# Performance work log

Measured on AMD Instinct MI355X. Metric: run time of the kernel, lower is better.

## Reference

```python
import jax, jax.numpy as jnp
import numpy as np

K = 4096          # in_features
N = 11008         # out_features
GROUP = 128       # scale group size along K
PACK = 16
BATCH, SEQ = 2, 4096


def setup_inputs() -> dict:
    key = jax.random.key(0)
    k1, k2, k3, k4 = jax.random.split(key, 4)
    x = jax.random.normal(k1, (BATCH, SEQ, K), dtype=jnp.float16)
    # valid ternary codes in {0,1,2} encoding w = code - 1 in {-1,0,+1}
    codes = jax.random.randint(k2, (K, N), 0, 3, dtype=jnp.int32)
    codes = codes.reshape(K // PACK, PACK, N)
    shifts = (2 * jnp.arange(PACK, dtype=jnp.int32))[None, :, None]
    packed_weight = jnp.sum(codes << shifts, axis=1).astype(jnp.int32)  # (K//16, N)
    scales = (jax.random.uniform(k3, (K // GROUP, N), dtype=jnp.float32) * 0.1 + 0.01).astype(jnp.float16)
    bias = (jax.random.normal(k4, (N,), dtype=jnp.float32) * 0.01).astype(jnp.float16)
    return {"x": x, "packed_weight": packed_weight, "scales": scales, "bias": bias}


def _dequant(packed_weight, scales):
    # unpack 16 two-bit codes per int32 along K
    shifts = (2 * jnp.arange(PACK, dtype=jnp.int32))[None, :, None]
    codes = (packed_weight[:, None, :] >> shifts) & 3        # (K//16, 16, N)
    Kp = packed_weight.shape[0] * PACK
    Nn = packed_weight.shape[1]
    w = (codes.astype(jnp.float16) - jnp.float16(1.0)).reshape(Kp, Nn)  # ternary {-1,0,1}
    scale_full = jnp.repeat(scales, GROUP, axis=0)            # (K, N) group-wise gamma
    return w * scale_full


def reference(x, packed_weight, scales, bias):
    Kp = packed_weight.shape[0] * PACK
    Nn = packed_weight.shape[1]
    w = _dequant(packed_weight, scales)                       # (K, N) fp16
    x2 = x.reshape(-1, Kp).astype(jnp.float16)                # (M, K)
    out = jnp.dot(x2, w, preferred_element_type=jnp.float32).astype(jnp.float16)
    out = out + bias
    return out.reshape(*x.shape[:-1], Nn)
```

## Files before the change

kernel.cpp:

```cpp
#include <hip/hip_runtime.h>
#include <stdint.h>

#define K_DIM 4096
#define N_DIM 11008
#define M_DIM 8192
#define BM 256
#define BN 128
#define BK 64
#define NSLAB (K_DIM / BK)
#define NBN (N_DIM / BN)
#define NBM (M_DIM / BM)
#define NWG (NBN * NBM)
#define ABUF (BM * BK)

#define FBM 128
#define FBK 32
#define FASTRIDE 32
#define FBSTRIDE 40

typedef _Float16 half8   __attribute__((ext_vector_type(8)));
typedef _Float16 half2v  __attribute__((ext_vector_type(2)));
typedef float    floatx4 __attribute__((ext_vector_type(4)));

#define WS_NEEDED ((size_t)M_DIM * K_DIM * 2)

__device__ __forceinline__ void async_lds16(const void* g, void* l) {
    __builtin_amdgcn_global_load_lds(
        (const __attribute__((address_space(1))) uint32_t*)g,
        (__attribute__((address_space(3))) uint32_t*)l, 16, 0, 0);
}

__global__ __launch_bounds__(256) void cvt_a(const float* __restrict__ x,
                                             _Float16* __restrict__ xh) {
    const size_t i = ((size_t)blockIdx.x * 256 + threadIdx.x) * 8;
    const float4 a = *(const float4*)(x + i);
    const float4 b = *(const float4*)(x + i + 4);
    half8 h;
    h[0] = (_Float16)a.x; h[1] = (_Float16)a.y; h[2] = (_Float16)a.z; h[3] = (_Float16)a.w;
    h[4] = (_Float16)b.x; h[5] = (_Float16)b.y; h[6] = (_Float16)b.z; h[7] = (_Float16)b.w;
    *(half8*)(xh + i) = h;
}

__global__ __launch_bounds__(512, 4) void ternary_gemm_p2(
    const _Float16* __restrict__ xh,
    const int*   __restrict__ pw,
    const float* __restrict__ scales,
    const float* __restrict__ bias,
    float*       __restrict__ out)
{
    __shared__ __align__(16) _Float16 lds_a[2 * ABUF];
    __shared__ __align__(16) _Float16 lds_b[BN * BK];

    const int tid  = threadIdx.x;
    const int lane = tid & 63;
    const int w    = tid >> 6;

    const int bid = blockIdx.x;
    const int swz = (bid & 7) * (NWG / 8) + (bid >> 3);
    const int m0 = (swz / NBN) * BM;
    const int n0 = (swz % NBN) * BN;

    const int band = (w & 3) * 64;
    const int wn   = (w >> 2) * 64;

    const _Float16* ga[4];
    int laOff[4];
    #pragma unroll
    for (int i = 0; i < 4; ++i) {
        const int idx = tid + i * 512;
        const int row = idx >> 3;
        const int c   = idx & 7;
        ga[i]    = xh + (size_t)(m0 + row) * K_DIM + ((c ^ (row & 7)) * 8);
        laOff[i] = idx * 8;
    }

    const int nb = tid >> 2;
    const int kp = tid & 3;
    const int* pwp = pw + (size_t)kp * N_DIM + n0 + nb;
    const float* scp = scales + n0 + nb;
    const int s7 = nb & 7;
    const int cA = (kp * 2 + 0) ^ s7;
    const int cB = (kp * 2 + 1) ^ s7;
    _Float16* bl = lds_b + nb * BK;

    floatx4 acc[4][4];
    #pragma unroll
    for (int i = 0; i < 4; ++i)
        #pragma unroll
        for (int j = 0; j < 4; ++j)
            acc[i][j] = floatx4{0.f, 0.f, 0.f, 0.f};

    const int lr = lane & 15;
    const int g  = lane >> 4;
    const int x7 = lr & 7;

    int aoff[4], boff[4];
    #pragma unroll
    for (int t = 0; t < 4; ++t) {
        aoff[t] = (band + t * 16 + lr) * BK;
        boff[t] = (wn   + t * 16 + lr) * BK;
    }

    auto stage_a = [&](int t, int buf) {
        #pragma unroll
        for (int i = 0; i < 4; ++i)
            async_lds16(ga[i] + t * BK, lds_a + buf * ABUF + laOff[i]);
    };
    auto stage_b = [&](uint32_t v, float scf) {
        _Float16 sh = (_Float16)scf;
        uint32_t sbits = (uint32_t)__builtin_bit_cast(unsigned short, sh);
        uint32_t tmpl = sbits | (((sbits >> 8) ^ 0x80u) << 24);
        uint32_t q[8];
        #pragma unroll
        for (int j = 0; j < 8; ++j) {
            uint32_t t4 = (v >> (4 * j)) & 0xFu;
            uint32_t sp = (t4 | (t4 << 14)) & 0x00030003u;
            uint32_t sel = ((sp & 0x00010001u) << 1) | ((0x00030003u - sp) << 8);
            q[j] = __builtin_amdgcn_perm(tmpl, tmpl, sel);
        }
        *(uint4*)(bl + cA * 8) = make_uint4(q[0], q[1], q[2], q[3]);
        *(uint4*)(bl + cB * 8) = make_uint4(q[4], q[5], q[6], q[7]);
    };

    stage_a(0, 0);
    uint32_t pv0 = (uint32_t)pwp[0];
    float    sv0 = scp[0];
    uint32_t pv1 = (uint32_t)pwp[(size_t)4 * N_DIM];
    float    sv1 = scp[0];

    for (int t = 0; t < NSLAB; ++t) {
        const int cur = t & 1;

        if (t + 1 < NSLAB) stage_a(t + 1, cur ^ 1);
        uint32_t pv2 = 0; float sv2 = 0.f;
        if (t + 2 < NSLAB) {
            pv2 = (uint32_t)pwp[(size_t)(t + 2) * 4 * N_DIM];
            sv2 = scp[(size_t)((t + 2) >> 1) * N_DIM];
        }
        stage_b(pv0, sv0);

        if (t + 2 < NSLAB)      asm volatile("s_waitcnt vmcnt(6)" ::: "memory");
        else if (t + 1 < NSLAB) asm volatile("s_waitcnt vmcnt(4)" ::: "memory");
        else                    asm volatile("s_waitcnt vmcnt(0)" ::: "memory");
        asm volatile("s_waitcnt lgkmcnt(0)" ::: "memory");
        __builtin_amdgcn_sched_barrier(0);
        __builtin_amdgcn_s_barrier();

        const _Float16* Ab = lds_a + cur * ABUF;
        __builtin_amdgcn_s_setprio(1);
        #pragma unroll
        for (int h = 0; h < 2; ++h) {
            const int co = ((h * 4 + g) ^ x7) * 8;
            half8 af[4], bfr[4];
            #pragma unroll
            for (int tt = 0; tt < 4; ++tt) {
                af[tt]  = *(const half8*)&Ab[aoff[tt] + co];
                bfr[tt] = *(const half8*)&lds_b[boff[tt] + co];
            }
            #pragma unroll
            for (int mt = 0; mt < 4; ++mt)
                #pragma unroll
                for (int nt = 0; nt < 4; ++nt)
                    acc[mt][nt] = __builtin_amdgcn_mfma_f32_16x16x32_f16(
                        af[mt], bfr[nt], acc[mt][nt], 0, 0, 0);
        }
        __builtin_amdgcn_s_setprio(0);

        asm volatile("s_waitcnt lgkmcnt(0)" ::: "memory");
        __builtin_amdgcn_sched_barrier(0);
        __builtin_amdgcn_s_barrier();

        pv0 = pv1; sv0 = sv1; pv1 = pv2; sv1 = sv2;
    }

    float bv[4];
    #pragma unroll
    for (int nt = 0; nt < 4; ++nt) bv[nt] = bias[n0 + wn + nt * 16 + lr];

    const int rbase = g * 4;
    #pragma unroll
    for (int mt = 0; mt < 4; ++mt) {
        #pragma unroll
        for (int nt = 0; nt < 4; ++nt) {
            const int col = n0 + wn + nt * 16 + lr;
            float* op = out + (size_t)(m0 + band + mt * 16 + rbase) * N_DIM + col;
            floatx4 a = acc[mt][nt];
            #pragma unroll
            for (int r = 0; r < 4; ++r)
                op[(size_t)r * N_DIM] = a[r] + bv[nt];
        }
    }
}

__global__ __launch_bounds__(256, 2) void ternary_gemm(
    const float* __restrict__ x,
    const int*   __restrict__ pw,
    const float* __restrict__ scales,
    const float* __restrict__ bias,
    float*       __restrict__ out)
{
    __shared__ __align__(16) _Float16 lds_a[FBM * FASTRIDE];
    __shared__ __align__(16) _Float16 lds_b[FBM * FBSTRIDE];

    const int tid  = threadIdx.x;
    const int lane = tid & 63;
    const int wave = tid >> 6;

    const int n0 = blockIdx.x * FBM;
    const int m0 = blockIdx.y * FBM;

    const int wm = (wave & 1) * 64;
    const int wn = (wave >> 1) * 64;

    const int nb  = tid & 127;
    const int kpi = tid >> 7;
    const int*   pwp = pw + (size_t)kpi * N_DIM + n0 + nb;
    const float* scp = scales + n0 + nb;
    _Float16* bl = lds_b + nb * FBSTRIDE + kpi * 16;

    floatx4 acc[4][4];
    #pragma unroll
    for (int i = 0; i < 4; ++i)
        #pragma unroll
        for (int j = 0; j < 4; ++j)
            acc[i][j] = floatx4{0.f, 0.f, 0.f, 0.f};

    const int lr = lane & 15;
    const int qk = (lane >> 4) * 8;

    for (int slab = 0; slab < K_DIM / FBK; ++slab) {
        const int k0 = slab * FBK;

        #pragma unroll
        for (int i = 0; i < 4; ++i) {
            const int idx = tid + i * 256;
            const int row = idx >> 3;
            const int kq  = (idx & 7) * 4;
            float4 v4 = *(const float4*)(x + (size_t)(m0 + row) * K_DIM + k0 + kq);
            half2v h0; h0[0] = (_Float16)v4.x; h0[1] = (_Float16)v4.y;
            half2v h1; h1[0] = (_Float16)v4.z; h1[1] = (_Float16)v4.w;
            *(uint2*)(lds_a + row * FASTRIDE + kq) =
                make_uint2(__builtin_bit_cast(uint32_t, h0),
                           __builtin_bit_cast(uint32_t, h1));
        }

        uint32_t v  = (uint32_t)pwp[(size_t)slab * 2 * N_DIM];
        _Float16 sh = (_Float16)scp[(size_t)(slab >> 2) * N_DIM];
        uint32_t sbits = (uint32_t)__builtin_bit_cast(unsigned short, sh);
        uint32_t tmpl = sbits | (((sbits >> 8) ^ 0x80u) << 24);

        uint32_t q[8];
        #pragma unroll
        for (int j = 0; j < 8; ++j) {
            uint32_t t4 = (v >> (4 * j)) & 0xFu;
            uint32_t sp = (t4 | (t4 << 14)) & 0x00030003u;
            uint32_t sel = ((sp & 0x00010001u) << 1) | ((0x00030003u - sp) << 8);
            q[j] = __builtin_amdgcn_perm(tmpl, tmpl, sel);
        }
        *(uint4*)(bl)     = make_uint4(q[0], q[1], q[2], q[3]);
        *(uint4*)(bl + 8) = make_uint4(q[4], q[5], q[6], q[7]);

        __syncthreads();

        half8 af[4], bfr[4];
        #pragma unroll
        for (int t = 0; t < 4; ++t) {
            af[t]  = *(const half8*)&lds_a[(wm + t * 16 + lr) * FASTRIDE + qk];
            bfr[t] = *(const half8*)&lds_b[(wn + t * 16 + lr) * FBSTRIDE + qk];
        }
        #pragma unroll
        for (int mt = 0; mt < 4; ++mt)
            #pragma unroll
            for (int nt = 0; nt < 4; ++nt)
                acc[mt][nt] = __builtin_amdgcn_mfma_f32_16x16x32_f16(
                    af[mt], bfr[nt], acc[mt][nt], 0, 0, 0);

        __syncthreads();
    }

    float bv[4];
    #pragma unroll
    for (int nt = 0; nt < 4; ++nt) bv[nt] = bias[n0 + wn + nt * 16 + lr];

    const int rbase = (lane >> 4) * 4;
    #pragma unroll
    for (int mt = 0; mt < 4; ++mt) {
        #pragma unroll
        for (int nt = 0; nt < 4; ++nt) {
            const int col = n0 + wn + nt * 16 + lr;
            float* op = out + (size_t)(m0 + wm + mt * 16 + rbase) * N_DIM + col;
            floatx4 a = acc[mt][nt];
            #pragma unroll
            for (int r = 0; r < 4; ++r)
                op[(size_t)r * N_DIM] = a[r] + bv[nt];
        }
    }
}

extern "C" void kernel_launch(void* const* d_in, const int* in_sizes, int n_in,
                              void* d_out, int out_size, void* d_ws, size_t ws_size,
                              hipStream_t stream) {
    const float* x  = (const float*)d_in[0];
    const int*   pw = (const int*)d_in[1];
    const float* sc = (const float*)d_in[2];
    const float* bs = (const float*)d_in[3];
    float* out = (float*)d_out;

    if (d_ws != nullptr && ws_size >= WS_NEEDED) {
        _Float16* xh = (_Float16*)d_ws;
        cvt_a<<<dim3((unsigned)((size_t)M_DIM * K_DIM / (256 * 8))), 256, 0, stream>>>(x, xh);
        ternary_gemm_p2<<<dim3(NWG), 512, 0, stream>>>(xh, pw, sc, bs, out);
    } else {
        ternary_gemm<<<dim3(N_DIM / FBM, M_DIM / FBM), 256, 0, stream>>>(x, pw, sc, bs, out);
    }
}
```

Measured before the change: 1.070 ms.

## Halve workgroup size to 4 waves with 128x64 per-wave tiles

The main GEMM kernel now runs with 256 threads (4 waves) instead of 512 (8 waves) on the same 256x128 block tile. Each wave now computes a 128x64 sub-tile with 32 accumulators instead of 16, and each thread issues twice as many A async loads and dequantizes two packed words per slab. The goal is more MFMA work per LDS fragment load and fewer waves contending at barriers. The cost is much higher register pressure (128 accumulator VGPRs plus 12 fragments) and lower occupancy, with adjusted vmcnt waits.

```diff
diff --git a/kernel.cpp b/kernel.cpp
--- a/kernel.cpp
+++ b/kernel.cpp
@@ -41,7 +41,7 @@
     *(half8*)(xh + i) = h;
 }
 
-__global__ __launch_bounds__(512, 4) void ternary_gemm_p2(
+__global__ __launch_bounds__(256, 2) void ternary_gemm_w2(
     const _Float16* __restrict__ xh,
     const int*   __restrict__ pw,
     const float* __restrict__ scales,
@@ -60,32 +60,28 @@
     const int m0 = (swz / NBN) * BM;
     const int n0 = (swz % NBN) * BN;
 
-    const int band = (w & 3) * 64;
-    const int wn   = (w >> 2) * 64;
-
-    const _Float16* ga[4];
-    int laOff[4];
-    #pragma unroll
-    for (int i = 0; i < 4; ++i) {
-        const int idx = tid + i * 512;
-        const int row = idx >> 3;
-        const int c   = idx & 7;
-        ga[i]    = xh + (size_t)(m0 + row) * K_DIM + ((c ^ (row & 7)) * 8);
-        laOff[i] = idx * 8;
-    }
-
-    const int nb = tid >> 2;
-    const int kp = tid & 3;
-    const int* pwp = pw + (size_t)kp * N_DIM + n0 + nb;
+    const int band = (w >> 1) * 128;
+    const int wn   = (w & 1) * 64;
+
+    const int arow0 = tid >> 3;
+    const int achk  = (tid & 7) ^ (arow0 & 7);
+    const _Float16* gaBase = xh + (size_t)(m0 + arow0) * K_DIM + achk * 8;
+    const int laBase = tid * 8;
+
+    const int nb = tid >> 1;
+    const int kp = tid & 1;
+    const int* pwp = pw + (size_t)(kp * 2) * N_DIM + n0 + nb;
     const float* scp = scales + n0 + nb;
-    const int s7 = nb & 7;
-    const int cA = (kp * 2 + 0) ^ s7;
-    const int cB = (kp * 2 + 1) ^ s7;
+    const int s7  = nb & 7;
+    const int c0a = (kp * 4 + 0) ^ s7;
+    const int c0b = (kp * 4 + 1) ^ s7;
+    const int c1a = (kp * 4 + 2) ^ s7;
+    const int c1b = (kp * 4 + 3) ^ s7;
     _Float16* bl = lds_b + nb * BK;
 
-    floatx4 acc[4][4];
-    #pragma unroll
-    for (int i = 0; i < 4; ++i)
+    floatx4 acc[8][4];
+    #pragma unroll
+    for (int i = 0; i < 8; ++i)
         #pragma unroll
         for (int j = 0; j < 4; ++j)
             acc[i][j] = floatx4{0.f, 0.f, 0.f, 0.f};
@@ -94,23 +90,13 @@
     const int g  = lane >> 4;
     const int x7 = lr & 7;
 
-    int aoff[4], boff[4];
-    #pragma unroll
-    for (int t = 0; t < 4; ++t) {
-        aoff[t] = (band + t * 16 + lr) * BK;
-        boff[t] = (wn   + t * 16 + lr) * BK;
-    }
-
     auto stage_a = [&](int t, int buf) {
         #pragma unroll
-        for (int i = 0; i < 4; ++i)
-            async_lds16(ga[i] + t * BK, lds_a + buf * ABUF + laOff[i]);
+        for (int i = 0; i < 8; ++i)
+            async_lds16(gaBase + (size_t)i * 32 * K_DIM + t * BK,
+                        lds_a + buf * ABUF + laBase + i * 2048);
     };
-    auto stage_b = [&](uint32_t v, float scf) {
-        _Float16 sh = (_Float16)scf;
-        uint32_t sbits = (uint32_t)__builtin_bit_cast(unsigned short, sh);
-        uint32_t tmpl = sbits | (((sbits >> 8) ^ 0x80u) << 24);
-        uint32_t q[8];
+    auto permq = [](uint32_t v, uint32_t tmpl, uint32_t* q) {
         #pragma unroll
         for (int j = 0; j < 8; ++j) {
             uint32_t t4 = (v >> (4 * j)) & 0xFu;
@@ -118,30 +104,49 @@
             uint32_t sel = ((sp & 0x00010001u) << 1) | ((0x00030003u - sp) << 8);
             q[j] = __builtin_amdgcn_perm(tmpl, tmpl, sel);
         }
-        *(uint4*)(bl + cA * 8) = make_uint4(q[0], q[1], q[2], q[3]);
-        *(uint4*)(bl + cB * 8) = make_uint4(q[4], q[5], q[6], q[7]);
     };
+    auto stage_b = [&](uint32_t v0, uint32_t v1, float scf) {
+        _Float16 sh = (_Float16)scf;
+        uint32_t sbits = (uint32_t)__builtin_bit_cast(unsigned short, sh);
+        uint32_t tmpl = sbits | (((sbits >> 8) ^ 0x80u) << 24);
+        uint32_t q[8];
+        permq(v0, tmpl, q);
+        *(uint4*)(bl + c0a * 8) = make_uint4(q[0], q[1], q[2], q[3]);
+        *(uint4*)(bl + c0b * 8) = make_uint4(q[4], q[5], q[6], q[7]);
+        permq(v1, tmpl, q);
+        *(uint4*)(bl + c1a * 8) = make_uint4(q[0], q[1], q[2], q[3]);
+        *(uint4*)(bl + c1b * 8) = make_uint4(q[4], q[5], q[6], q[7]);
+    };
 
     stage_a(0, 0);
-    uint32_t pv0 = (uint32_t)pwp[0];
-    float    sv0 = scp[0];
-    uint32_t pv1 = (uint32_t)pwp[(size_t)4 * N_DIM];
-    float    sv1 = scp[0];
+    uint32_t pv0a = (uint32_t)pwp[0];
+    uint32_t pv0b = (uint32_t)pwp[(size_t)1 * N_DIM];
+    float    sv0  = scp[0];
+    uint32_t pv1a = (uint32_t)pwp[(size_t)4 * N_DIM];
+    uint32_t pv1b = (uint32_t)pwp[(size_t)5 * N_DIM];
+    float    sv1  = scp[0];
+
+    int aoff[8], boff[4];
+    #pragma unroll
+    for (int t = 0; t < 8; ++t) aoff[t] = (band + t * 16 + lr) * BK;
+    #pragma unroll
+    for (int t = 0; t < 4; ++t) boff[t] = (wn + t * 16 + lr) * BK;
 
     for (int t = 0; t < NSLAB; ++t) {
         const int cur = t & 1;
 
         if (t + 1 < NSLAB) stage_a(t + 1, cur ^ 1);
-        uint32_t pv2 = 0; float sv2 = 0.f;
+        uint32_t pv2a = 0, pv2b = 0; float sv2 = 0.f;
         if (t + 2 < NSLAB) {
-            pv2 = (uint32_t)pwp[(size_t)(t + 2) * 4 * N_DIM];
-            sv2 = scp[(size_t)((t + 2) >> 1) * N_DIM];
-        }
-        stage_b(pv0, sv0);
-
-        if (t + 2 < NSLAB)      asm volatile("s_waitcnt vmcnt(6)" ::: "memory");
-        else if (t + 1 < NSLAB) asm volatile("s_waitcnt vmcnt(4)" ::: "memory");
-        else                    asm volatile("s_waitcnt vmcnt(0)" ::: "memory");
+            pv2a = (uint32_t)pwp[(size_t)((t + 2) * 4 + 0) * N_DIM];
+            pv2b = (uint32_t)pwp[(size_t)((t + 2) * 4 + 1) * N_DIM];
+            sv2  = scp[(size_t)((t + 2) >> 1) * N_DIM];
+        }
+        stage_b(pv0a, pv0b, sv0);
+
+        if (t + 2 < NSLAB)      asm volatile("s_waitcnt vmcnt(11)" ::: "memory");
+        else if (t + 1 < NSLAB) asm volatile("s_waitcnt vmcnt(8)"  ::: "memory");
+        else                    asm volatile("s_waitcnt vmcnt(0)"  ::: "memory");
         asm volatile("s_waitcnt lgkmcnt(0)" ::: "memory");
         __builtin_amdgcn_sched_barrier(0);
         __builtin_amdgcn_s_barrier();
@@ -151,14 +156,13 @@
         #pragma unroll
         for (int h = 0; h < 2; ++h) {
             const int co = ((h * 4 + g) ^ x7) * 8;
-            half8 af[4], bfr[4];
-            #pragma unroll
-            for (int tt = 0; tt < 4; ++tt) {
-                af[tt]  = *(const half8*)&Ab[aoff[tt] + co];
-                bfr[tt] = *(const half8*)&lds_b[boff[tt] + co];
-            }
-            #pragma unroll
-            for (int mt = 0; mt < 4; ++mt)
+            half8 af[8], bfr[4];
+            #pragma unroll
+            for (int tt = 0; tt < 8; ++tt) af[tt]  = *(const half8*)&Ab[aoff[tt] + co];
+            #pragma unroll
+            for (int tt = 0; tt < 4; ++tt) bfr[tt] = *(const half8*)&lds_b[boff[tt] + co];
+            #pragma unroll
+            for (int mt = 0; mt < 8; ++mt)
                 #pragma unroll
                 for (int nt = 0; nt < 4; ++nt)
                     acc[mt][nt] = __builtin_amdgcn_mfma_f32_16x16x32_f16(
@@ -170,7 +174,8 @@
         __builtin_amdgcn_sched_barrier(0);
         __builtin_amdgcn_s_barrier();
 
-        pv0 = pv1; sv0 = sv1; pv1 = pv2; sv1 = sv2;
+        pv0a = pv1a; pv0b = pv1b; sv0 = sv1;
+        pv1a = pv2a; pv1b = pv2b; sv1 = sv2;
     }
 
     float bv[4];
@@ -179,7 +184,7 @@
 
     const int rbase = g * 4;
     #pragma unroll
-    for (int mt = 0; mt < 4; ++mt) {
+    for (int mt = 0; mt < 8; ++mt) {
         #pragma unroll
         for (int nt = 0; nt < 4; ++nt) {
             const int col = n0 + wn + nt * 16 + lr;
@@ -309,7 +314,7 @@
     if (d_ws != nullptr && ws_size >= WS_NEEDED) {
         _Float16* xh = (_Float16*)d_ws;
         cvt_a<<<dim3((unsigned)((size_t)M_DIM * K_DIM / (256 * 8))), 256, 0, stream>>>(x, xh);
-        ternary_gemm_p2<<<dim3(NWG), 512, 0, stream>>>(xh, pw, sc, bs, out);
+        ternary_gemm_w2<<<dim3(NWG), 256, 0, stream>>>(xh, pw, sc, bs, out);
     } else {
         ternary_gemm<<<dim3(N_DIM / FBM, M_DIM / FBM), 256, 0, stream>>>(x, pw, sc, bs, out);
     }
```

Result: no change. 1.078 ms (+0.8%).

## Triple-buffer A slabs with BK=32 and double-buffer B to drop a barrier

Applied to the files above, without the earlier changes.

Halves the A K-slab to 32 and keeps three A buffers in LDS, so the slab two steps ahead is in flight while the current one is consumed. The dequantised B tile stays 64 wide but is now double-buffered and refilled every other step. Each iteration keeps only a single workgroup barrier instead of two, and the A swizzle is reworked for the narrower rows. The intent is to remove the second barrier and expose more load-compute overlap. In exchange, each iteration does half the MFMA work between barriers, and the vmcnt bookkeeping is more delicate.

```diff
diff --git a/kernel.cpp b/kernel.cpp
--- a/kernel.cpp
+++ b/kernel.cpp
@@ -6,12 +6,14 @@
 #define M_DIM 8192
 #define BM 256
 #define BN 128
-#define BK 64
+#define BK 32
 #define NSLAB (K_DIM / BK)
+#define NPAIR (NSLAB / 2)
 #define NBN (N_DIM / BN)
 #define NBM (M_DIM / BM)
 #define NWG (NBN * NBM)
-#define ABUF (BM * BK)
+#define AQ (BM * BK)
+#define BH (BN * 64)
 
 #define FBM 128
 #define FBK 32
@@ -41,15 +43,15 @@
     *(half8*)(xh + i) = h;
 }
 
-__global__ __launch_bounds__(512, 4) void ternary_gemm_p2(
+__global__ __launch_bounds__(512, 4) void ternary_gemm_r3(
     const _Float16* __restrict__ xh,
     const int*   __restrict__ pw,
     const float* __restrict__ scales,
     const float* __restrict__ bias,
     float*       __restrict__ out)
 {
-    __shared__ __align__(16) _Float16 lds_a[2 * ABUF];
-    __shared__ __align__(16) _Float16 lds_b[BN * BK];
+    __shared__ __align__(16) _Float16 lds_a[3 * AQ];
+    __shared__ __align__(16) _Float16 lds_b[2 * BH];
 
     const int tid  = threadIdx.x;
     const int lane = tid & 63;
@@ -63,15 +65,15 @@
     const int band = (w & 3) * 64;
     const int wn   = (w >> 2) * 64;
 
-    const _Float16* ga[4];
-    int laOff[4];
-    #pragma unroll
-    for (int i = 0; i < 4; ++i) {
+    const _Float16* gaS[2];
+    int laO[2];
+    #pragma unroll
+    for (int i = 0; i < 2; ++i) {
         const int idx = tid + i * 512;
-        const int row = idx >> 3;
-        const int c   = idx & 7;
-        ga[i]    = xh + (size_t)(m0 + row) * K_DIM + ((c ^ (row & 7)) * 8);
-        laOff[i] = idx * 8;
+        const int row = idx >> 2;
+        const int c   = idx & 3;
+        gaS[i] = xh + (size_t)(m0 + row) * K_DIM + ((c ^ ((row >> 1) & 3)) * 8);
+        laO[i] = idx * 8;
     }
 
     const int nb = tid >> 2;
@@ -81,7 +83,6 @@
     const int s7 = nb & 7;
     const int cA = (kp * 2 + 0) ^ s7;
     const int cB = (kp * 2 + 1) ^ s7;
-    _Float16* bl = lds_b + nb * BK;
 
     floatx4 acc[4][4];
     #pragma unroll
@@ -94,19 +95,22 @@
     const int g  = lane >> 4;
     const int x7 = lr & 7;
 
-    int aoff[4], boff[4];
+    int aoff[4], boff[4], bsl[2];
     #pragma unroll
     for (int t = 0; t < 4; ++t) {
-        aoff[t] = (band + t * 16 + lr) * BK;
-        boff[t] = (wn   + t * 16 + lr) * BK;
-    }
+        aoff[t] = (band + t * 16 + lr) * BK + ((g ^ ((lr >> 1) & 3)) * 8);
+        boff[t] = (wn + t * 16 + lr) * 64;
+    }
+    bsl[0] = ((0 * 4 + g) ^ x7) * 8;
+    bsl[1] = ((1 * 4 + g) ^ x7) * 8;
 
     auto stage_a = [&](int t, int buf) {
         #pragma unroll
-        for (int i = 0; i < 4; ++i)
-            async_lds16(ga[i] + t * BK, lds_a + buf * ABUF + laOff[i]);
+        for (int i = 0; i < 2; ++i)
+            async_lds16(gaS[i] + t * BK, lds_a + buf * AQ + laO[i]);
     };
-    auto stage_b = [&](uint32_t v, float scf) {
+    auto stage_b = [&](uint32_t v, float scf, int half) {
+        _Float16* rowb = lds_b + half * BH + nb * 64;
         _Float16 sh = (_Float16)scf;
         uint32_t sbits = (uint32_t)__builtin_bit_cast(unsigned short, sh);
         uint32_t tmpl = sbits | (((sbits >> 8) ^ 0x80u) << 24);
@@ -118,59 +122,67 @@
             uint32_t sel = ((sp & 0x00010001u) << 1) | ((0x00030003u - sp) << 8);
             q[j] = __builtin_amdgcn_perm(tmpl, tmpl, sel);
         }
-        *(uint4*)(bl + cA * 8) = make_uint4(q[0], q[1], q[2], q[3]);
-        *(uint4*)(bl + cB * 8) = make_uint4(q[4], q[5], q[6], q[7]);
+        *(uint4*)(rowb + cA * 8) = make_uint4(q[0], q[1], q[2], q[3]);
+        *(uint4*)(rowb + cB * 8) = make_uint4(q[4], q[5], q[6], q[7]);
     };
 
-    stage_a(0, 0);
-    uint32_t pv0 = (uint32_t)pwp[0];
-    float    sv0 = scp[0];
-    uint32_t pv1 = (uint32_t)pwp[(size_t)4 * N_DIM];
-    float    sv1 = scp[0];
+    uint32_t pvP1; float svP1;
+    {
+        uint32_t pv0 = (uint32_t)pwp[0];
+        float    sv0 = scp[0];
+        pvP1 = (uint32_t)pwp[(size_t)4 * N_DIM];
+        svP1 = scp[0];
+        stage_a(0, 0);
+        stage_a(1, 1);
+        stage_b(pv0, sv0, 0);
+    }
+    uint32_t pvP2 = 0; float svP2 = 0.f;
+
+    int rcur = 0, rstg = 2;
 
     for (int t = 0; t < NSLAB; ++t) {
-        const int cur = t & 1;
-
-        if (t + 1 < NSLAB) stage_a(t + 1, cur ^ 1);
-        uint32_t pv2 = 0; float sv2 = 0.f;
-        if (t + 2 < NSLAB) {
-            pv2 = (uint32_t)pwp[(size_t)(t + 2) * 4 * N_DIM];
-            sv2 = scp[(size_t)((t + 2) >> 1) * N_DIM];
-        }
-        stage_b(pv0, sv0);
-
-        if (t + 2 < NSLAB)      asm volatile("s_waitcnt vmcnt(6)" ::: "memory");
-        else if (t + 1 < NSLAB) asm volatile("s_waitcnt vmcnt(4)" ::: "memory");
-        else                    asm volatile("s_waitcnt vmcnt(0)" ::: "memory");
+        if (t >= NSLAB - 2)      asm volatile("s_waitcnt vmcnt(0)" ::: "memory");
+        else if ((t & 1) && t != NSLAB - 3)
+                                 asm volatile("s_waitcnt vmcnt(4)" ::: "memory");
+        else                     asm volatile("s_waitcnt vmcnt(2)" ::: "memory");
         asm volatile("s_waitcnt lgkmcnt(0)" ::: "memory");
         __builtin_amdgcn_sched_barrier(0);
         __builtin_amdgcn_s_barrier();
-
-        const _Float16* Ab = lds_a + cur * ABUF;
+        __builtin_amdgcn_sched_barrier(0);
+
+        if (!(t & 1)) {
+            const int p = t >> 1;
+            if (p + 2 < NPAIR) {
+                pvP2 = (uint32_t)pwp[(size_t)(p + 2) * 4 * N_DIM];
+                svP2 = scp[(size_t)((p + 2) >> 1) * N_DIM];
+            }
+        }
+        if (t + 2 < NSLAB) stage_a(t + 2, rstg);
+        if (!(t & 1)) {
+            const int p = t >> 1;
+            if (p + 1 < NPAIR) stage_b(pvP1, svP1, (p + 1) & 1);
+        }
+
+        const _Float16* Ab = lds_a + rcur * AQ;
+        const _Float16* Bb = lds_b + ((t >> 1) & 1) * BH;
+        const int bs = bsl[t & 1];
         __builtin_amdgcn_s_setprio(1);
-        #pragma unroll
-        for (int h = 0; h < 2; ++h) {
-            const int co = ((h * 4 + g) ^ x7) * 8;
-            half8 af[4], bfr[4];
+        half8 af[4], bf[4];
+        #pragma unroll
+        for (int tt = 0; tt < 4; ++tt) af[tt] = *(const half8*)&Ab[aoff[tt]];
+        #pragma unroll
+        for (int tt = 0; tt < 4; ++tt) bf[tt] = *(const half8*)&Bb[boff[tt] + bs];
+        #pragma unroll
+        for (int mt = 0; mt < 4; ++mt)
             #pragma unroll
-            for (int tt = 0; tt < 4; ++tt) {
-                af[tt]  = *(const half8*)&Ab[aoff[tt] + co];
-                bfr[tt] = *(const half8*)&lds_b[boff[tt] + co];
-            }
-            #pragma unroll
-            for (int mt = 0; mt < 4; ++mt)
-                #pragma unroll
-                for (int nt = 0; nt < 4; ++nt)
-                    acc[mt][nt] = __builtin_amdgcn_mfma_f32_16x16x32_f16(
-                        af[mt], bfr[nt], acc[mt][nt], 0, 0, 0);
-        }
+            for (int nt = 0; nt < 4; ++nt)
+                acc[mt][nt] = __builtin_amdgcn_mfma_f32_16x16x32_f16(
+                    af[mt], bf[nt], acc[mt][nt], 0, 0, 0);
         __builtin_amdgcn_s_setprio(0);
 
-        asm volatile("s_waitcnt lgkmcnt(0)" ::: "memory");
-        __builtin_amdgcn_sched_barrier(0);
-        __builtin_amdgcn_s_barrier();
-
-        pv0 = pv1; sv0 = sv1; pv1 = pv2; sv1 = sv2;
+        if (t & 1) { pvP1 = pvP2; svP1 = svP2; }
+        rcur = (rcur == 2) ? 0 : rcur + 1;
+        rstg = (rstg == 2) ? 0 : rstg + 1;
     }
 
     float bv[4];
@@ -309,7 +321,7 @@
     if (d_ws != nullptr && ws_size >= WS_NEEDED) {
         _Float16* xh = (_Float16*)d_ws;
         cvt_a<<<dim3((unsigned)((size_t)M_DIM * K_DIM / (256 * 8))), 256, 0, stream>>>(x, xh);
-        ternary_gemm_p2<<<dim3(NWG), 512, 0, stream>>>(xh, pw, sc, bs, out);
+        ternary_gemm_r3<<<dim3(NWG), 512, 0, stream>>>(xh, pw, sc, bs, out);
     } else {
         ternary_gemm<<<dim3(N_DIM / FBM, M_DIM / FBM), 256, 0, stream>>>(x, pw, sc, bs, out);
     }
```

Result: slower. 1.146 ms (+7.1%).
